# Optimization experiments

Hardware: AMD Instinct MI355X
Metric: run time of the kernel (lower is better)

## Reference

```python
import jax, jax.numpy as jnp
import numpy as np

NUM_LABELS = 64
START, END, PAD = 0, 1, 2
B, L, V, D = 128, 1024, 30000, 256


def make_transitions(key):
    # replicates CRF.init_weights
    t = jax.random.uniform(key, (NUM_LABELS, NUM_LABELS), minval=-0.1, maxval=0.1)
    t = t.at[:, START].set(-10000.0)
    t = t.at[END, :].set(-10000.0)
    t = t.at[PAD, :].set(-10000.0)
    t = t.at[:, PAD].set(-10000.0)
    t = t.at[PAD, PAD].set(0.0)
    t = t.at[PAD, END].set(0.0)
    return t.astype(jnp.float32)


def setup_inputs() -> dict:
    key = jax.random.key(0)
    k0, k1, k2, k3, k4 = jax.random.split(key, 5)
    x = jax.random.randint(k0, (B, L), 0, V)
    tags = jax.random.randint(k1, (B, L), 0, NUM_LABELS)
    mask = jnp.ones((B, L), dtype=jnp.float32)  # ignored by CRF (source passes mask=None)
    embed = jax.random.normal(k2, (V, D), dtype=jnp.float32)
    W = jax.random.normal(k3, (D, NUM_LABELS), dtype=jnp.float32) * 0.05
    b = jnp.zeros((NUM_LABELS,), dtype=jnp.float32)
    trans = make_transitions(k4)
    return {"x": x, "tags": tags, "mask": mask, "embed": embed, "W": W, "b": b, "trans": trans}


def _crf_nll(emissions, tags, trans):
    # emissions: [B, L, T]; tags: [B, L]; trans: [T, T]
    # NOTE: original CRF.forward ignores the user mask (passes mask=None ->
    # all-ones mask), so every position is valid and last tag is tags[:, -1].
    # gold path score
    e_scores = jnp.take_along_axis(emissions, tags[:, :, None], axis=2)[:, :, 0].sum(axis=1)
    t_scores = trans[tags[:, :-1], tags[:, 1:]].sum(axis=1)
    scores = e_scores + t_scores + trans[START, tags[:, 0]] + trans[tags[:, -1], END]
    # log partition: forward algorithm (log-space recursion over time)
    alpha0 = trans[START][None, :] + emissions[:, 0]  # [B, T]

    def step(alphas, emit_t):
        # alphas: [B, T_prev] -> logsumexp over previous tag
        new = jax.nn.logsumexp(alphas[:, :, None] + trans[None, :, :], axis=1) + emit_t
        return new, None

    alphas, _ = jax.lax.scan(step, alpha0, jnp.swapaxes(emissions[:, 1:], 0, 1))
    log_z = jax.nn.logsumexp(alphas + trans[:, END][None, :], axis=1)  # [B]
    return -jnp.sum(scores - log_z)


def reference(x, tags, mask, embed, W, b, trans):
    emissions = embed[x] @ W + b  # [B, L, T]
    return _crf_nll(emissions, tags, trans)
```

## Files before the change

### kernel.cpp

```cpp
#include <hip/hip_runtime.h>
#include <hip/hip_bf16.h>

#define B_ 128
#define L_ 1024
#define T_ 64
#define CSH 5
#define C_ 32

using short8 = __attribute__((ext_vector_type(8))) short;
using f32x4  = __attribute__((ext_vector_type(4))) float;
using f32x16 = __attribute__((ext_vector_type(16))) float;

static __device__ __forceinline__ unsigned short bfb(float x) {
  return __builtin_bit_cast(unsigned short, __float2bfloat16(x));
}
static __device__ __forceinline__ float asf(unsigned u) { return __builtin_bit_cast(float, u); }
static __device__ __forceinline__ float bf2f(unsigned short b) { return asf(((unsigned)b) << 16); }
static __device__ __forceinline__ unsigned pk2(float lo, float hi) {
  __hip_bfloat162 h = __float22bfloat162_rn(float2{lo, hi});
  unsigned u;
  __builtin_memcpy(&u, &h, 4);
  return u;
}
static __device__ __forceinline__ unsigned pk2t(float lo, float hi) {
  return __builtin_amdgcn_perm(__builtin_bit_cast(unsigned, hi),
                               __builtin_bit_cast(unsigned, lo), 0x07060302u);
}
static __device__ __forceinline__ void pswap(unsigned& x, unsigned& y) {
  asm("v_permlane32_swap_b32 %0, %1" : "+v"(x), "+v"(y));
}

__global__ __launch_bounds__(256) void k_prep(const float* __restrict__ W,
                                              unsigned short* __restrict__ Wswz,
                                              float* __restrict__ score,
                                              float* __restrict__ out) {
  if (blockIdx.x == 0) {
    if (threadIdx.x < 128) score[threadIdx.x] = 0.f;
    if (threadIdx.x == 0) out[0] = 0.f;
  }
  const int t = blockIdx.x * 256 + threadIdx.x;
  const int e = t * 4, k = e >> 6, n0 = e & 63;
  float4 w4 = *(const float4*)(W + e);
  const int base = ((k >> 5) << 11) + ((n0 >> 4) << 9) + (((k >> 3) & 3) << 7) +
                   ((n0 & 15) << 3) + (k & 7);
  Wswz[base + 0]  = bfb(w4.x);
  Wswz[base + 8]  = bfb(w4.y);
  Wswz[base + 16] = bfb(w4.z);
  Wswz[base + 24] = bfb(w4.w);
}

__global__ __launch_bounds__(256) void k_scan(const int* __restrict__ x,
                                              const int* __restrict__ tags,
                                              const float* __restrict__ embed,
                                              const unsigned short* __restrict__ Wswz,
                                              const float* __restrict__ bias,
                                              const float* __restrict__ trans,
                                              uint4* __restrict__ XT,
                                              float* __restrict__ rlog,
                                              float* __restrict__ score) {
  __shared__ __align__(16) unsigned short Ftile[4][2048];
  const int wv = threadIdx.x >> 6, L = threadIdx.x & 63;
  const int job = blockIdx.x * 4 + wv;
  const int c = job & (C_ - 1);
  const int b = job >> CSH;
  const int K = (1023 + C_ - 1) >> CSH;
  const int a = 1 + c * K;
  const int len = min(K, 1024 - a);
  const int nh = L & 31, hh = L >> 5;
  const int m = L & 15, q = L >> 4;
  unsigned short* Ft = Ftile[wv];
  const int* tg = tags + (size_t)b * L_;

  const float bj0 = bias[m], bj1 = bias[16 + m], bj2 = bias[32 + m], bj3 = bias[48 + m];
  for (int p = 0; p < 2; p++) {
    int tok = a + 16 * p + m;
    if (tok > 1023) tok = 1023;
    const float* er = embed + (size_t)x[b * 1024 + tok] * 256;
    f32x4 acc[4] = {{0.f,0.f,0.f,0.f},{0.f,0.f,0.f,0.f},{0.f,0.f,0.f,0.f},{0.f,0.f,0.f,0.f}};
#pragma unroll
    for (int kap = 0; kap < 8; kap++) {
      float4 p0 = *(const float4*)(er + 32 * kap + 8 * q);
      float4 p1 = *(const float4*)(er + 32 * kap + 8 * q + 4);
      unsigned u0 = pk2(p0.x, p0.y), u1 = pk2(p0.z, p0.w);
      unsigned u2 = pk2(p1.x, p1.y), u3 = pk2(p1.z, p1.w);
      short8 af = __builtin_bit_cast(short8, make_uint4(u0, u1, u2, u3));
#pragma unroll
      for (int u = 0; u < 4; u++) {
        short8 bf8 = *(const short8*)&Wswz[kap * 2048 + u * 512 + q * 128 + m * 8];
        acc[u] = __builtin_amdgcn_mfma_f32_16x16x32_bf16(af, bf8, acc[u], 0, 0, 0);
      }
    }
#pragma unroll
    for (int r = 0; r < 4; r++) {
      float e0 = acc[0][r] + bj0, e1 = acc[1][r] + bj1;
      float e2 = acc[2][r] + bj2, e3 = acc[3][r] + bj3;
      float mr = fmaxf(fmaxf(e0, e1), fmaxf(e2, e3));
#pragma unroll
      for (int off = 1; off < 16; off <<= 1) mr = fmaxf(mr, __shfl_xor(mr, off));
      float x0 = __expf(e0 - mr), x1 = __expf(e1 - mr);
      float x2 = __expf(e2 - mr), x3 = __expf(e3 - mr);
      float sr = (x0 + x1) + (x2 + x3);
#pragma unroll
      for (int off = 1; off < 16; off <<= 1) sr += __shfl_xor(sr, off);
      float rs = 1.0f / sr;
      const int row = 16 * p + 4 * q + r;
      Ft[row * 64 + m]      = bfb(x0 * rs);
      Ft[row * 64 + 16 + m] = bfb(x1 * rs);
      Ft[row * 64 + 32 + m] = bfb(x2 * rs);
      Ft[row * 64 + 48 + m] = bfb(x3 * rs);
    }
  }
  {
    float gold = 0.f;
    if (L < len) {
      const int tga = tg[a + L], tgp = tg[a - 1 + L];
      gold = __logf(bf2f(Ft[L * 64 + tga])) + trans[tgp * T_ + tga];
    }
#pragma unroll
    for (int off = 1; off < 64; off <<= 1) gold += __shfl_xor(gold, off);
    if (L == 0) atomicAdd(&score[b], gold);
  }

  short8 Af[2][4];
#pragma unroll
  for (int I = 0; I < 2; I++)
#pragma unroll
    for (int kap = 0; kap < 4; kap++) {
      short8 aa;
#pragma unroll
      for (int d = 0; d < 8; d++) {
        const int k = 16 * kap + 8 * hh + d;
        aa[d] = (short)bfb(__expf(trans[k * T_ + 32 * I + nh]));
      }
      Af[I][kap] = aa;
    }
  unsigned Bf[4][2][4];
#pragma unroll
  for (int kap = 0; kap < 4; kap++)
#pragma unroll
    for (int J = 0; J < 2; J++)
#pragma unroll
      for (int dw = 0; dw < 4; dw++) {
        int k0 = 16 * kap + 8 * hh + 2 * dw, n = 32 * J + nh;
        unsigned u = 0;
        if (k0 == n) u = 0x3F80u;
        if (k0 + 1 == n) u = 0x3F800000u;
        Bf[kap][J][dw] = u;
      }

  float logacc = 0.f;
  const f32x16 Z = {};
  for (int s = 0; s < len; s++) {
    uint2 Fc[2][4];
#pragma unroll
    for (int I = 0; I < 2; I++)
#pragma unroll
      for (int j = 0; j < 4; j++)
        Fc[I][j] = *(const uint2*)&Ft[s * 64 + (16 * I + 4 * j + 2 * hh) * 2];
    const bool rn = ((s & 15) == 15);
    float rs = 1.0f;
#pragma unroll
    for (int J = 0; J < 2; J++) {
      f32x16 D[2];
#pragma unroll
      for (int I = 0; I < 2; I++) {
        short8 b0 = __builtin_bit_cast(short8,
            make_uint4(Bf[0][J][0], Bf[0][J][1], Bf[0][J][2], Bf[0][J][3]));
        f32x16 d = __builtin_amdgcn_mfma_f32_32x32x16_bf16(Af[I][0], b0, Z, 0, 0, 0);
#pragma unroll
        for (int kap = 1; kap < 4; kap++) {
          short8 bk = __builtin_bit_cast(short8,
              make_uint4(Bf[kap][J][0], Bf[kap][J][1], Bf[kap][J][2], Bf[kap][J][3]));
          d = __builtin_amdgcn_mfma_f32_32x32x16_bf16(Af[I][kap], bk, d, 0, 0, 0);
        }
        D[I] = d;
      }
#pragma unroll
      for (int I = 0; I < 2; I++)
#pragma unroll
        for (int j = 0; j < 4; j++) {
          uint2 g = Fc[I][j];
          float f0 = asf(g.x << 16), f1 = asf(g.x & 0xffff0000u);
          float f2 = asf(g.y << 16), f3 = asf(g.y & 0xffff0000u);
          D[I][4 * j + 0] *= f0;
          D[I][4 * j + 1] *= f1;
          D[I][4 * j + 2] *= f2;
          D[I][4 * j + 3] *= f3;
        }
      if (rn) {
        if (J == 0) {
          float mx = D[0][0];
#pragma unroll
          for (int I = 0; I < 2; I++)
#pragma unroll
            for (int r = 0; r < 16; r++) mx = fmaxf(mx, D[I][r]);
#pragma unroll
          for (int off = 1; off < 64; off <<= 1) mx = fmaxf(mx, __shfl_xor(mx, off));
          rs = 1.0f / mx;
          logacc += __logf(mx);
        }
#pragma unroll
        for (int I = 0; I < 2; I++)
#pragma unroll
          for (int r = 0; r < 16; r++) D[I][r] *= rs;
      }
      unsigned PDt[2][4][2];
#pragma unroll
      for (int I = 0; I < 2; I++)
#pragma unroll
        for (int j = 0; j < 4; j++) {
          PDt[I][j][0] = pk2t(D[I][4 * j + 0], D[I][4 * j + 1]);
          PDt[I][j][1] = pk2t(D[I][4 * j + 2], D[I][4 * j + 3]);
        }
#pragma unroll
      for (int kap = 0; kap < 4; kap++) {
        const int Ip = kap >> 1, e2 = 2 * (kap & 1);
        unsigned x0 = PDt[Ip][e2][0], y0 = PDt[Ip][e2 + 1][0];
        unsigned x1 = PDt[Ip][e2][1], y1 = PDt[Ip][e2 + 1][1];
        pswap(x0, y0);
        pswap(x1, y1);
        Bf[kap][J][0] = x0;
        Bf[kap][J][1] = x1;
        Bf[kap][J][2] = y0;
        Bf[kap][J][3] = y1;
      }
    }
  }
  {
    uint4* Xj = XT + (size_t)job * 512 + L;
#pragma unroll
    for (int J = 0; J < 2; J++)
#pragma unroll
      for (int kap = 0; kap < 4; kap++)
        Xj[(J * 4 + kap) * 64] =
            make_uint4(Bf[kap][J][0], Bf[kap][J][1], Bf[kap][J][2], Bf[kap][J][3]);
  }
  if (L == 0) rlog[job] = logacc;
}

__global__ __launch_bounds__(256) void k_tail(const uint4* __restrict__ XT,
                                              const float* __restrict__ rlog,
                                              const float* __restrict__ score,
                                              const int* __restrict__ x,
                                              const float* __restrict__ embed,
                                              const float* __restrict__ W,
                                              const float* __restrict__ bias,
                                              const float* __restrict__ trans,
                                              const int* __restrict__ tags,
                                              float* __restrict__ out) {
  __shared__ __align__(16) unsigned short Ptile[4][4096];
  __shared__ __align__(16) float vS[64];
  __shared__ float tlg[4];
  const int wv = threadIdx.x >> 6, L = threadIdx.x & 63;
  const int b = blockIdx.x;
  const int nh = L & 31, hh = L >> 5;
  const int* tg = tags + (size_t)b * L_;
  const f32x16 Z = {};
  unsigned Bf[4][2][4];

  const uint4* Sb4 = XT + ((size_t)(b * C_ + 8 * wv)) * 512 + L;
  {
    float plog = 0.f;
#pragma unroll
    for (int kap = 0; kap < 4; kap++)
#pragma unroll
      for (int J = 0; J < 2; J++)
#pragma unroll
        for (int dw = 0; dw < 4; dw++) {
          int k0 = 16 * kap + 8 * hh + 2 * dw, n = 32 * J + nh;
          unsigned u = 0;
          if (k0 == n) u = 0x3F80u;
          if (k0 + 1 == n) u = 0x3F800000u;
          Bf[kap][J][dw] = u;
        }
    uint4 Aq[2][4], Aqn[2][4];
#pragma unroll
    for (int I = 0; I < 2; I++)
#pragma unroll
      for (int kap = 0; kap < 4; kap++)
        Aq[I][kap] = Sb4[7 * 512 + (I * 4 + kap) * 64];
    for (int rr = 0; rr < 8; rr++) {
      const int r = 7 - rr;
      if (r > 0) {
#pragma unroll
        for (int I = 0; I < 2; I++)
#pragma unroll
          for (int kap = 0; kap < 4; kap++)
            Aqn[I][kap] = Sb4[(size_t)(r - 1) * 512 + (I * 4 + kap) * 64];
      }
      short8 Ap[2][4];
#pragma unroll
      for (int I = 0; I < 2; I++)
#pragma unroll
        for (int kap = 0; kap < 4; kap++)
          Ap[I][kap] = __builtin_bit_cast(short8, Aq[I][kap]);
      const bool last = (r == 0);
      float rsw = 1.0f;
#pragma unroll
      for (int J = 0; J < 2; J++) {
        f32x16 D[2];
#pragma unroll
        for (int I = 0; I < 2; I++) {
          short8 b0 = __builtin_bit_cast(short8,
              make_uint4(Bf[0][J][0], Bf[0][J][1], Bf[0][J][2], Bf[0][J][3]));
          f32x16 d = __builtin_amdgcn_mfma_f32_32x32x16_bf16(Ap[I][0], b0, Z, 0, 0, 0);
#pragma unroll
          for (int kap = 1; kap < 4; kap++) {
            short8 bk = __builtin_bit_cast(short8,
                make_uint4(Bf[kap][J][0], Bf[kap][J][1], Bf[kap][J][2], Bf[kap][J][3]));
            d = __builtin_amdgcn_mfma_f32_32x32x16_bf16(Ap[I][kap], bk, d, 0, 0, 0);
          }
          D[I] = d;
        }
        if (J == 0) {
          float mx = D[0][0];
#pragma unroll
          for (int I = 0; I < 2; I++)
#pragma unroll
            for (int rr2 = 0; rr2 < 16; rr2++) mx = fmaxf(mx, D[I][rr2]);
#pragma unroll
          for (int off = 1; off < 64; off <<= 1) mx = fmaxf(mx, __shfl_xor(mx, off));
          mx = fmaxf(mx, 1e-30f);
          rsw = 1.0f / mx;
          plog += __logf(mx);
        }
#pragma unroll
        for (int I = 0; I < 2; I++)
#pragma unroll
          for (int rr2 = 0; rr2 < 16; rr2++) D[I][rr2] *= rsw;
        unsigned PDt[2][4][2];
#pragma unroll
        for (int I = 0; I < 2; I++)
#pragma unroll
          for (int j = 0; j < 4; j++) {
            PDt[I][j][0] = pk2t(D[I][4 * j + 0], D[I][4 * j + 1]);
            PDt[I][j][1] = pk2t(D[I][4 * j + 2], D[I][4 * j + 3]);
          }
        if (last) {
          unsigned short* Xrow = Ptile[wv] + 32 * J + nh;
#pragma unroll
          for (int I = 0; I < 2; I++)
#pragma unroll
            for (int j = 0; j < 4; j++)
#pragma unroll
              for (int pp = 0; pp < 2; pp++) {
                const int rw = 32 * I + 8 * j + 4 * hh + 2 * pp;
                Xrow[rw * 64] = (unsigned short)(PDt[I][j][pp] & 0xffffu);
                Xrow[(rw + 1) * 64] = (unsigned short)(PDt[I][j][pp] >> 16);
              }
        } else {
#pragma unroll
          for (int kap = 0; kap < 4; kap++) {
            const int Ip = kap >> 1, e2 = 2 * (kap & 1);
            unsigned x0 = PDt[Ip][e2][0], y0 = PDt[Ip][e2 + 1][0];
            unsigned x1 = PDt[Ip][e2][1], y1 = PDt[Ip][e2 + 1][1];
            pswap(x0, y0);
            pswap(x1, y1);
            Bf[kap][J][0] = x0;
            Bf[kap][J][1] = x1;
            Bf[kap][J][2] = y0;
            Bf[kap][J][3] = y1;
          }
        }
      }
      if (r > 0) {
#pragma unroll
        for (int I = 0; I < 2; I++)
#pragma unroll
          for (int kap = 0; kap < 4; kap++)
            Aq[I][kap] = Aqn[I][kap];
      }
    }
    if (L == 0) tlg[wv] = plog;
  }
  __syncthreads();
  if (threadIdx.x >= 64) return;

  float tlog = (tlg[0] + tlg[1]) + (tlg[2] + tlg[3]);

  const int i = L;
  const float* er0 = embed + (size_t)x[(size_t)b * L_] * 256;
  float e0 = bias[i], e1 = 0.f, e2 = 0.f, e3 = 0.f;
#pragma unroll 16
  for (int d = 0; d < 256; d += 4) {
    e0 = fmaf(er0[d + 0], W[(d + 0) * T_ + i], e0);
    e1 = fmaf(er0[d + 1], W[(d + 1) * T_ + i], e1);
    e2 = fmaf(er0[d + 2], W[(d + 2) * T_ + i], e2);
    e3 = fmaf(er0[d + 3], W[(d + 3) * T_ + i], e3);
  }
  float e = (e0 + e1) + (e2 + e3);
  float mr = e;
#pragma unroll
  for (int off = 1; off < 64; off <<= 1) mr = fmaxf(mr, __shfl_xor(mr, off));
  float pex = __expf(e - mr);
  float sr = pex;
#pragma unroll
  for (int off = 1; off < 64; off <<= 1) sr += __shfl_xor(sr, off);
  const int t0 = tg[0];
  float sc = score[b];
  sc += (__shfl(e, t0) - mr) - __logf(sr);
  sc += trans[t0] + trans[tg[L_ - 1] * T_ + 1];
  vS[i] = __expf(trans[i]) * (pex / sr);
  float rl = (i < 32) ? rlog[b * C_ + i] : 0.f;
#pragma unroll
  for (int off = 1; off < 64; off <<= 1) rl += __shfl_xor(rl, off);

  float tacc = 0.f;
  {
#pragma unroll
    for (int kap = 0; kap < 4; kap++)
#pragma unroll
      for (int J = 0; J < 2; J++)
#pragma unroll
        for (int dw = 0; dw < 4; dw++) {
          int k0 = 16 * kap + 8 * hh + 2 * dw, n = 32 * J + nh;
          unsigned u = 0;
          if (k0 == n) u = 0x3F80u;
          if (k0 + 1 == n) u = 0x3F800000u;
          Bf[kap][J][dw] = u;
        }
    for (int rr = 0; rr < 4; rr++) {
      const int r = 3 - rr;
      short8 Ap[2][4];
#pragma unroll
      for (int I = 0; I < 2; I++)
#pragma unroll
        for (int kap = 0; kap < 4; kap++)
          Ap[I][kap] = *(const short8*)&Ptile[r][(32 * I + nh) * 64 + 16 * kap + 8 * hh];
      const bool last = (r == 0);
      float rsw = 1.0f;
#pragma unroll
      for (int J = 0; J < 2; J++) {
        f32x16 D[2];
#pragma unroll
        for (int I = 0; I < 2; I++) {
          short8 b0 = __builtin_bit_cast(short8,
              make_uint4(Bf[0][J][0], Bf[0][J][1], Bf[0][J][2], Bf[0][J][3]));
          f32x16 d = __builtin_amdgcn_mfma_f32_32x32x16_bf16(Ap[I][0], b0, Z, 0, 0, 0);
#pragma unroll
          for (int kap = 1; kap < 4; kap++) {
            short8 bk = __builtin_bit_cast(short8,
                make_uint4(Bf[kap][J][0], Bf[kap][J][1], Bf[kap][J][2], Bf[kap][J][3]));
            d = __builtin_amdgcn_mfma_f32_32x32x16_bf16(Ap[I][kap], bk, d, 0, 0, 0);
          }
          D[I] = d;
        }
        if (J == 0) {
          float mx = D[0][0];
#pragma unroll
          for (int I = 0; I < 2; I++)
#pragma unroll
            for (int rr2 = 0; rr2 < 16; rr2++) mx = fmaxf(mx, D[I][rr2]);
#pragma unroll
          for (int off = 1; off < 64; off <<= 1) mx = fmaxf(mx, __shfl_xor(mx, off));
          mx = fmaxf(mx, 1e-30f);
          rsw = 1.0f / mx;
          tlog += __logf(mx);
        }
#pragma unroll
        for (int I = 0; I < 2; I++)
#pragma unroll
          for (int rr2 = 0; rr2 < 16; rr2++) D[I][rr2] *= rsw;
        if (last) {
          float dJ = 0.f;
#pragma unroll
          for (int I = 0; I < 2; I++)
#pragma unroll
            for (int r2 = 0; r2 < 16; r2++)
              dJ = fmaf(D[I][r2], vS[32 * I + (r2 & 3) + 8 * (r2 >> 2) + 4 * hh], dJ);
          tacc = fmaf(__expf(trans[(32 * J + nh) * T_ + 1]), dJ, tacc);
        } else {
          unsigned PDt[2][4][2];
#pragma unroll
          for (int I = 0; I < 2; I++)
#pragma unroll
            for (int j = 0; j < 4; j++) {
              PDt[I][j][0] = pk2t(D[I][4 * j + 0], D[I][4 * j + 1]);
              PDt[I][j][1] = pk2t(D[I][4 * j + 2], D[I][4 * j + 3]);
            }
#pragma unroll
          for (int kap = 0; kap < 4; kap++) {
            const int Ip = kap >> 1, e2b = 2 * (kap & 1);
            unsigned x0 = PDt[Ip][e2b][0], y0 = PDt[Ip][e2b + 1][0];
            unsigned x1 = PDt[Ip][e2b][1], y1 = PDt[Ip][e2b + 1][1];
            pswap(x0, y0);
            pswap(x1, y1);
            Bf[kap][J][0] = x0;
            Bf[kap][J][1] = x1;
            Bf[kap][J][2] = y0;
            Bf[kap][J][3] = y1;
          }
        }
      }
    }
  }
  float t2 = tacc;
#pragma unroll
  for (int off = 1; off < 64; off <<= 1) t2 += __shfl_xor(t2, off);
  if (i == 0) {
    const float logz = rl + tlog + __logf(t2);
    atomicAdd(out, -(sc - logz));
  }
}

extern "C" void kernel_launch(void* const* d_in, const int* in_sizes, int n_in,
                              void* d_out, int out_size, void* d_ws, size_t ws_size,
                              hipStream_t stream) {
  const int* x = (const int*)d_in[0];
  const int* tags = (const int*)d_in[1];
  const float* embed = (const float*)d_in[3];
  const float* W = (const float*)d_in[4];
  const float* bias = (const float*)d_in[5];
  const float* trans = (const float*)d_in[6];

  char* ws = (char*)d_ws;
  uint4* XT = (uint4*)ws;
  float* rlog = (float*)(ws + (size_t)C_ * 1048576);
  float* score = (float*)((char*)rlog + 4096 * 4);
  unsigned short* Wswz = (unsigned short*)((char*)score + 128 * 4);
  float* out = (float*)d_out;

  k_prep<<<16, 256, 0, stream>>>(W, Wswz, score, out);
  k_scan<<<32 * C_, 256, 0, stream>>>(x, tags, embed, Wswz, bias, trans, XT, rlog, score);
  k_tail<<<B_, 256, 0, stream>>>(XT, rlog, score, x, embed, W, bias, trans, tags, out);
}
```

Measured before the change: 191.7 us.

## Split each scan chunk across two waves by output column half

Each chunk job of the forward-algorithm matrix chain now runs on a 128-thread block with two waves. Each wave computes one 32-column half of the 64x64 product, where before a single wave did both halves serially. The emission tile is built cooperatively, one 16-token half per wave. The periodic renormalisation scale is shared through LDS with a block barrier every 16 steps. This halves the per-wave serial MFMA chain length and doubles the number of waves, at the cost of barrier synchronisation and some duplicated work per wave.

Result: no change. 192.3 us (+0.3%).

```diff
diff --git a/kernel.cpp b/kernel.cpp
--- a/kernel.cpp
+++ b/kernel.cpp
@@ -49,7 +49,7 @@
   Wswz[base + 24] = bfb(w4.w);
 }
 
-__global__ __launch_bounds__(256) void k_scan(const int* __restrict__ x,
+__global__ __launch_bounds__(128) void k_scan(const int* __restrict__ x,
                                               const int* __restrict__ tags,
                                               const float* __restrict__ embed,
                                               const unsigned short* __restrict__ Wswz,
@@ -58,9 +58,10 @@
                                               uint4* __restrict__ XT,
                                               float* __restrict__ rlog,
                                               float* __restrict__ score) {
-  __shared__ __align__(16) unsigned short Ftile[4][2048];
+  __shared__ __align__(16) unsigned short Ftile[2048];
+  __shared__ float rsx[2];
   const int wv = threadIdx.x >> 6, L = threadIdx.x & 63;
-  const int job = blockIdx.x * 4 + wv;
+  const int job = blockIdx.x;
   const int c = job & (C_ - 1);
   const int b = job >> CSH;
   const int K = (1023 + C_ - 1) >> CSH;
@@ -68,11 +69,12 @@
   const int len = min(K, 1024 - a);
   const int nh = L & 31, hh = L >> 5;
   const int m = L & 15, q = L >> 4;
-  unsigned short* Ft = Ftile[wv];
+  unsigned short* Ft = Ftile;
   const int* tg = tags + (size_t)b * L_;
 
   const float bj0 = bias[m], bj1 = bias[16 + m], bj2 = bias[32 + m], bj3 = bias[48 + m];
-  for (int p = 0; p < 2; p++) {
+  {
+    const int p = wv;
     int tok = a + 16 * p + m;
     if (tok > 1023) tok = 1023;
     const float* er = embed + (size_t)x[b * 1024 + tok] * 256;
@@ -110,7 +112,8 @@
       Ft[row * 64 + 48 + m] = bfb(x3 * rs);
     }
   }
-  {
+  __syncthreads();
+  if (wv == 0) {
     float gold = 0.f;
     if (L < len) {
       const int tga = tg[a + L], tgp = tg[a - 1 + L];
@@ -134,19 +137,17 @@
       }
       Af[I][kap] = aa;
     }
-  unsigned Bf[4][2][4];
+  unsigned Bf[4][4];
 #pragma unroll
   for (int kap = 0; kap < 4; kap++)
 #pragma unroll
-    for (int J = 0; J < 2; J++)
-#pragma unroll
-      for (int dw = 0; dw < 4; dw++) {
-        int k0 = 16 * kap + 8 * hh + 2 * dw, n = 32 * J + nh;
-        unsigned u = 0;
-        if (k0 == n) u = 0x3F80u;
-        if (k0 + 1 == n) u = 0x3F800000u;
-        Bf[kap][J][dw] = u;
-      }
+    for (int dw = 0; dw < 4; dw++) {
+      int k0 = 16 * kap + 8 * hh + 2 * dw, n = 32 * wv + nh;
+      unsigned u = 0;
+      if (k0 == n) u = 0x3F80u;
+      if (k0 + 1 == n) u = 0x3F800000u;
+      Bf[kap][dw] = u;
+    }
 
   float logacc = 0.f;
   const f32x16 Z = {};
@@ -158,84 +159,80 @@
       for (int j = 0; j < 4; j++)
         Fc[I][j] = *(const uint2*)&Ft[s * 64 + (16 * I + 4 * j + 2 * hh) * 2];
     const bool rn = ((s & 15) == 15);
-    float rs = 1.0f;
-#pragma unroll
-    for (int J = 0; J < 2; J++) {
-      f32x16 D[2];
-#pragma unroll
-      for (int I = 0; I < 2; I++) {
-        short8 b0 = __builtin_bit_cast(short8,
-            make_uint4(Bf[0][J][0], Bf[0][J][1], Bf[0][J][2], Bf[0][J][3]));
-        f32x16 d = __builtin_amdgcn_mfma_f32_32x32x16_bf16(Af[I][0], b0, Z, 0, 0, 0);
-#pragma unroll
-        for (int kap = 1; kap < 4; kap++) {
-          short8 bk = __builtin_bit_cast(short8,
-              make_uint4(Bf[kap][J][0], Bf[kap][J][1], Bf[kap][J][2], Bf[kap][J][3]));
-          d = __builtin_amdgcn_mfma_f32_32x32x16_bf16(Af[I][kap], bk, d, 0, 0, 0);
-        }
-        D[I] = d;
-      }
+    f32x16 D[2];
+#pragma unroll
+    for (int I = 0; I < 2; I++) {
+      short8 b0 = __builtin_bit_cast(short8,
+          make_uint4(Bf[0][0], Bf[0][1], Bf[0][2], Bf[0][3]));
+      f32x16 d = __builtin_amdgcn_mfma_f32_32x32x16_bf16(Af[I][0], b0, Z, 0, 0, 0);
+#pragma unroll
+      for (int kap = 1; kap < 4; kap++) {
+        short8 bk = __builtin_bit_cast(short8,
+            make_uint4(Bf[kap][0], Bf[kap][1], Bf[kap][2], Bf[kap][3]));
+        d = __builtin_amdgcn_mfma_f32_32x32x16_bf16(Af[I][kap], bk, d, 0, 0, 0);
+      }
+      D[I] = d;
+    }
+#pragma unroll
+    for (int I = 0; I < 2; I++)
+#pragma unroll
+      for (int j = 0; j < 4; j++) {
+        uint2 g = Fc[I][j];
+        float f0 = asf(g.x << 16), f1 = asf(g.x & 0xffff0000u);
+        float f2 = asf(g.y << 16), f3 = asf(g.y & 0xffff0000u);
+        D[I][4 * j + 0] *= f0;
+        D[I][4 * j + 1] *= f1;
+        D[I][4 * j + 2] *= f2;
+        D[I][4 * j + 3] *= f3;
+      }
+    if (rn) {
+      if (wv == 0) {
+        float mx = D[0][0];
+#pragma unroll
+        for (int I = 0; I < 2; I++)
+#pragma unroll
+          for (int r = 0; r < 16; r++) mx = fmaxf(mx, D[I][r]);
+#pragma unroll
+        for (int off = 1; off < 64; off <<= 1) mx = fmaxf(mx, __shfl_xor(mx, off));
+        logacc += __logf(mx);
+        rsx[(s >> 4) & 1] = 1.0f / mx;
+      }
+      __syncthreads();
+      const float rs = rsx[(s >> 4) & 1];
 #pragma unroll
       for (int I = 0; I < 2; I++)
 #pragma unroll
-        for (int j = 0; j < 4; j++) {
-          uint2 g = Fc[I][j];
-          float f0 = asf(g.x << 16), f1 = asf(g.x & 0xffff0000u);
-          float f2 = asf(g.y << 16), f3 = asf(g.y & 0xffff0000u);
-          D[I][4 * j + 0] *= f0;
-          D[I][4 * j + 1] *= f1;
-          D[I][4 * j + 2] *= f2;
-          D[I][4 * j + 3] *= f3;
-        }
-      if (rn) {
-        if (J == 0) {
-          float mx = D[0][0];
-#pragma unroll
-          for (int I = 0; I < 2; I++)
-#pragma unroll
-            for (int r = 0; r < 16; r++) mx = fmaxf(mx, D[I][r]);
-#pragma unroll
-          for (int off = 1; off < 64; off <<= 1) mx = fmaxf(mx, __shfl_xor(mx, off));
-          rs = 1.0f / mx;
-          logacc += __logf(mx);
-        }
-#pragma unroll
-        for (int I = 0; I < 2; I++)
-#pragma unroll
-          for (int r = 0; r < 16; r++) D[I][r] *= rs;
-      }
-      unsigned PDt[2][4][2];
-#pragma unroll
-      for (int I = 0; I < 2; I++)
-#pragma unroll
-        for (int j = 0; j < 4; j++) {
-          PDt[I][j][0] = pk2t(D[I][4 * j + 0], D[I][4 * j + 1]);
-          PDt[I][j][1] = pk2t(D[I][4 * j + 2], D[I][4 * j + 3]);
-        }
-#pragma unroll
-      for (int kap = 0; kap < 4; kap++) {
-        const int Ip = kap >> 1, e2 = 2 * (kap & 1);
-        unsigned x0 = PDt[Ip][e2][0], y0 = PDt[Ip][e2 + 1][0];
-        unsigned x1 = PDt[Ip][e2][1], y1 = PDt[Ip][e2 + 1][1];
-        pswap(x0, y0);
-        pswap(x1, y1);
-        Bf[kap][J][0] = x0;
-        Bf[kap][J][1] = x1;
-        Bf[kap][J][2] = y0;
-        Bf[kap][J][3] = y1;
-      }
+        for (int r = 0; r < 16; r++) D[I][r] *= rs;
+    }
+    unsigned PDt[2][4][2];
+#pragma unroll
+    for (int I = 0; I < 2; I++)
+#pragma unroll
+      for (int j = 0; j < 4; j++) {
+        PDt[I][j][0] = pk2t(D[I][4 * j + 0], D[I][4 * j + 1]);
+        PDt[I][j][1] = pk2t(D[I][4 * j + 2], D[I][4 * j + 3]);
+      }
+#pragma unroll
+    for (int kap = 0; kap < 4; kap++) {
+      const int Ip = kap >> 1, e2 = 2 * (kap & 1);
+      unsigned x0 = PDt[Ip][e2][0], y0 = PDt[Ip][e2 + 1][0];
+      unsigned x1 = PDt[Ip][e2][1], y1 = PDt[Ip][e2 + 1][1];
+      pswap(x0, y0);
+      pswap(x1, y1);
+      Bf[kap][0] = x0;
+      Bf[kap][1] = x1;
+      Bf[kap][2] = y0;
+      Bf[kap][3] = y1;
     }
   }
   {
     uint4* Xj = XT + (size_t)job * 512 + L;
 #pragma unroll
-    for (int J = 0; J < 2; J++)
-#pragma unroll
-      for (int kap = 0; kap < 4; kap++)
-        Xj[(J * 4 + kap) * 64] =
-            make_uint4(Bf[kap][J][0], Bf[kap][J][1], Bf[kap][J][2], Bf[kap][J][3]);
-  }
-  if (L == 0) rlog[job] = logacc;
+    for (int kap = 0; kap < 4; kap++)
+      Xj[(wv * 4 + kap) * 64] =
+          make_uint4(Bf[kap][0], Bf[kap][1], Bf[kap][2], Bf[kap][3]);
+  }
+  if (wv == 0 && L == 0) rlog[job] = logacc;
 }
 
 __global__ __launch_bounds__(256) void k_tail(const uint4* __restrict__ XT,
@@ -521,6 +518,6 @@
   float* out = (float*)d_out;
 
   k_prep<<<16, 256, 0, stream>>>(W, Wswz, score, out);
-  k_scan<<<32 * C_, 256, 0, stream>>>(x, tags, embed, Wswz, bias, trans, XT, rlog, score);
+  k_scan<<<B_ * C_, 128, 0, stream>>>(x, tags, embed, Wswz, bias, trans, XT, rlog, score);
   k_tail<<<B_, 256, 0, stream>>>(XT, rlog, score, x, embed, W, bias, trans, tags, out);
 }
```

## Process two independent chunk scans per wavefront to interleave MFMA chains

Applied to the files above, without the earlier changes.

Each wavefront now handles two adjacent time chunks of the same sequence instead of one, interleaving their serial MFMA transfer-matrix recurrences in one loop. The two independent dependency chains are meant to hide MFMA and conversion latency in the latency-bound scan, and the grid shrinks by half. In exchange it roughly doubles register pressure, which may reduce occupancy or cause spills, and it adds a predicate for the shorter final chunk.

Result: slower. 238.0 us (+24.1%).

```diff
diff --git a/kernel.cpp b/kernel.cpp
--- a/kernel.cpp
+++ b/kernel.cpp
@@ -58,63 +58,73 @@
                                               uint4* __restrict__ XT,
                                               float* __restrict__ rlog,
                                               float* __restrict__ score) {
-  __shared__ __align__(16) unsigned short Ftile[4][2048];
+  __shared__ __align__(16) unsigned short Ftile[4][2][2048];
   const int wv = threadIdx.x >> 6, L = threadIdx.x & 63;
-  const int job = blockIdx.x * 4 + wv;
-  const int c = job & (C_ - 1);
-  const int b = job >> CSH;
-  const int K = (1023 + C_ - 1) >> CSH;
-  const int a = 1 + c * K;
-  const int len = min(K, 1024 - a);
+  const int job0 = blockIdx.x * 8 + wv * 2;
+  const int job1 = job0 + 1;
+  const int c0 = job0 & (C_ - 1);
+  const int b = job0 >> CSH;
+  const int a0 = 1 + c0 * 32, a1 = a0 + 32;
+  const int len1 = min(32, 1024 - a1);
   const int nh = L & 31, hh = L >> 5;
   const int m = L & 15, q = L >> 4;
-  unsigned short* Ft = Ftile[wv];
+  unsigned short* Ft0 = Ftile[wv][0];
+  unsigned short* Ft1 = Ftile[wv][1];
   const int* tg = tags + (size_t)b * L_;
 
   const float bj0 = bias[m], bj1 = bias[16 + m], bj2 = bias[32 + m], bj3 = bias[48 + m];
-  for (int p = 0; p < 2; p++) {
-    int tok = a + 16 * p + m;
-    if (tok > 1023) tok = 1023;
-    const float* er = embed + (size_t)x[b * 1024 + tok] * 256;
-    f32x4 acc[4] = {{0.f,0.f,0.f,0.f},{0.f,0.f,0.f,0.f},{0.f,0.f,0.f,0.f},{0.f,0.f,0.f,0.f}};
-#pragma unroll
-    for (int kap = 0; kap < 8; kap++) {
-      float4 p0 = *(const float4*)(er + 32 * kap + 8 * q);
-      float4 p1 = *(const float4*)(er + 32 * kap + 8 * q + 4);
-      unsigned u0 = pk2(p0.x, p0.y), u1 = pk2(p0.z, p0.w);
-      unsigned u2 = pk2(p1.x, p1.y), u3 = pk2(p1.z, p1.w);
-      short8 af = __builtin_bit_cast(short8, make_uint4(u0, u1, u2, u3));
-#pragma unroll
-      for (int u = 0; u < 4; u++) {
-        short8 bf8 = *(const short8*)&Wswz[kap * 2048 + u * 512 + q * 128 + m * 8];
-        acc[u] = __builtin_amdgcn_mfma_f32_16x16x32_bf16(af, bf8, acc[u], 0, 0, 0);
-      }
-    }
-#pragma unroll
-    for (int r = 0; r < 4; r++) {
-      float e0 = acc[0][r] + bj0, e1 = acc[1][r] + bj1;
-      float e2 = acc[2][r] + bj2, e3 = acc[3][r] + bj3;
-      float mr = fmaxf(fmaxf(e0, e1), fmaxf(e2, e3));
-#pragma unroll
-      for (int off = 1; off < 16; off <<= 1) mr = fmaxf(mr, __shfl_xor(mr, off));
-      float x0 = __expf(e0 - mr), x1 = __expf(e1 - mr);
-      float x2 = __expf(e2 - mr), x3 = __expf(e3 - mr);
-      float sr = (x0 + x1) + (x2 + x3);
-#pragma unroll
-      for (int off = 1; off < 16; off <<= 1) sr += __shfl_xor(sr, off);
-      float rs = 1.0f / sr;
-      const int row = 16 * p + 4 * q + r;
-      Ft[row * 64 + m]      = bfb(x0 * rs);
-      Ft[row * 64 + 16 + m] = bfb(x1 * rs);
-      Ft[row * 64 + 32 + m] = bfb(x2 * rs);
-      Ft[row * 64 + 48 + m] = bfb(x3 * rs);
+#pragma unroll
+  for (int jb = 0; jb < 2; jb++) {
+    unsigned short* Ftj = jb ? Ft1 : Ft0;
+    const int aj = jb ? a1 : a0;
+    for (int p = 0; p < 2; p++) {
+      int tok = aj + 16 * p + m;
+      if (tok > 1023) tok = 1023;
+      const float* er = embed + (size_t)x[b * 1024 + tok] * 256;
+      f32x4 acc[4] = {{0.f,0.f,0.f,0.f},{0.f,0.f,0.f,0.f},{0.f,0.f,0.f,0.f},{0.f,0.f,0.f,0.f}};
+#pragma unroll
+      for (int kap = 0; kap < 8; kap++) {
+        float4 p0 = *(const float4*)(er + 32 * kap + 8 * q);
+        float4 p1 = *(const float4*)(er + 32 * kap + 8 * q + 4);
+        unsigned u0 = pk2(p0.x, p0.y), u1 = pk2(p0.z, p0.w);
+        unsigned u2 = pk2(p1.x, p1.y), u3 = pk2(p1.z, p1.w);
+        short8 af = __builtin_bit_cast(short8, make_uint4(u0, u1, u2, u3));
+#pragma unroll
+        for (int u = 0; u < 4; u++) {
+          short8 bf8 = *(const short8*)&Wswz[kap * 2048 + u * 512 + q * 128 + m * 8];
+          acc[u] = __builtin_amdgcn_mfma_f32_16x16x32_bf16(af, bf8, acc[u], 0, 0, 0);
+        }
+      }
+#pragma unroll
+      for (int r = 0; r < 4; r++) {
+        float e0 = acc[0][r] + bj0, e1 = acc[1][r] + bj1;
+        float e2 = acc[2][r] + bj2, e3 = acc[3][r] + bj3;
+        float mr = fmaxf(fmaxf(e0, e1), fmaxf(e2, e3));
+#pragma unroll
+        for (int off = 1; off < 16; off <<= 1) mr = fmaxf(mr, __shfl_xor(mr, off));
+        float x0 = __expf(e0 - mr), x1 = __expf(e1 - mr);
+        float x2 = __expf(e2 - mr), x3 = __expf(e3 - mr);
+        float sr = (x0 + x1) + (x2 + x3);
+#pragma unroll
+        for (int off = 1; off < 16; off <<= 1) sr += __shfl_xor(sr, off);
+        float rs = 1.0f / sr;
+        const int row = 16 * p + 4 * q + r;
+        Ftj[row * 64 + m]      = bfb(x0 * rs);
+        Ftj[row * 64 + 16 + m] = bfb(x1 * rs);
+        Ftj[row * 64 + 32 + m] = bfb(x2 * rs);
+        Ftj[row * 64 + 48 + m] = bfb(x3 * rs);
+      }
     }
   }
   {
     float gold = 0.f;
-    if (L < len) {
-      const int tga = tg[a + L], tgp = tg[a - 1 + L];
-      gold = __logf(bf2f(Ft[L * 64 + tga])) + trans[tgp * T_ + tga];
+    if (L < 32) {
+      const int tga = tg[a0 + L], tgp = tg[a0 - 1 + L];
+      gold += __logf(bf2f(Ft0[L * 64 + tga])) + trans[tgp * T_ + tga];
+    }
+    if (L < len1) {
+      const int tga = tg[a1 + L], tgp = tg[a1 - 1 + L];
+      gold += __logf(bf2f(Ft1[L * 64 + tga])) + trans[tgp * T_ + tga];
     }
 #pragma unroll
     for (int off = 1; off < 64; off <<= 1) gold += __shfl_xor(gold, off);
@@ -134,7 +144,7 @@
       }
       Af[I][kap] = aa;
     }
-  unsigned Bf[4][2][4];
+  unsigned Bf0[4][2][4], Bf1[4][2][4];
 #pragma unroll
   for (int kap = 0; kap < 4; kap++)
 #pragma unroll
@@ -145,97 +155,180 @@
         unsigned u = 0;
         if (k0 == n) u = 0x3F80u;
         if (k0 + 1 == n) u = 0x3F800000u;
-        Bf[kap][J][dw] = u;
-      }
-
-  float logacc = 0.f;
+        Bf0[kap][J][dw] = u;
+        Bf1[kap][J][dw] = u;
+      }
+
+  float logacc0 = 0.f, logacc1 = 0.f;
   const f32x16 Z = {};
-  for (int s = 0; s < len; s++) {
-    uint2 Fc[2][4];
+  for (int s = 0; s < 32; s++) {
+    const bool do1 = (s < len1);
+    const bool rn = ((s & 15) == 15);
+    uint2 Fc0[2][4], Fc1[2][4];
 #pragma unroll
     for (int I = 0; I < 2; I++)
 #pragma unroll
       for (int j = 0; j < 4; j++)
-        Fc[I][j] = *(const uint2*)&Ft[s * 64 + (16 * I + 4 * j + 2 * hh) * 2];
-    const bool rn = ((s & 15) == 15);
-    float rs = 1.0f;
+        Fc0[I][j] = *(const uint2*)&Ft0[s * 64 + (16 * I + 4 * j + 2 * hh) * 2];
+    if (do1) {
+#pragma unroll
+      for (int I = 0; I < 2; I++)
+#pragma unroll
+        for (int j = 0; j < 4; j++)
+          Fc1[I][j] = *(const uint2*)&Ft1[s * 64 + (16 * I + 4 * j + 2 * hh) * 2];
+    }
+    float rs0 = 1.0f, rs1 = 1.0f;
 #pragma unroll
     for (int J = 0; J < 2; J++) {
-      f32x16 D[2];
+      short8 bk0[4], bk1[4];
+#pragma unroll
+      for (int kap = 0; kap < 4; kap++)
+        bk0[kap] = __builtin_bit_cast(short8,
+            make_uint4(Bf0[kap][J][0], Bf0[kap][J][1], Bf0[kap][J][2], Bf0[kap][J][3]));
+      if (do1) {
+#pragma unroll
+        for (int kap = 0; kap < 4; kap++)
+          bk1[kap] = __builtin_bit_cast(short8,
+              make_uint4(Bf1[kap][J][0], Bf1[kap][J][1], Bf1[kap][J][2], Bf1[kap][J][3]));
+      }
+      f32x16 D0[2], D1[2];
 #pragma unroll
       for (int I = 0; I < 2; I++) {
-        short8 b0 = __builtin_bit_cast(short8,
-            make_uint4(Bf[0][J][0], Bf[0][J][1], Bf[0][J][2], Bf[0][J][3]));
-        f32x16 d = __builtin_amdgcn_mfma_f32_32x32x16_bf16(Af[I][0], b0, Z, 0, 0, 0);
-#pragma unroll
-        for (int kap = 1; kap < 4; kap++) {
-          short8 bk = __builtin_bit_cast(short8,
-              make_uint4(Bf[kap][J][0], Bf[kap][J][1], Bf[kap][J][2], Bf[kap][J][3]));
-          d = __builtin_amdgcn_mfma_f32_32x32x16_bf16(Af[I][kap], bk, d, 0, 0, 0);
-        }
-        D[I] = d;
+        f32x16 d = __builtin_amdgcn_mfma_f32_32x32x16_bf16(Af[I][0], bk0[0], Z, 0, 0, 0);
+#pragma unroll
+        for (int kap = 1; kap < 4; kap++)
+          d = __builtin_amdgcn_mfma_f32_32x32x16_bf16(Af[I][kap], bk0[kap], d, 0, 0, 0);
+        D0[I] = d;
+      }
+      if (do1) {
+#pragma unroll
+        for (int I = 0; I < 2; I++) {
+          f32x16 d = __builtin_amdgcn_mfma_f32_32x32x16_bf16(Af[I][0], bk1[0], Z, 0, 0, 0);
+#pragma unroll
+          for (int kap = 1; kap < 4; kap++)
+            d = __builtin_amdgcn_mfma_f32_32x32x16_bf16(Af[I][kap], bk1[kap], d, 0, 0, 0);
+          D1[I] = d;
+        }
       }
 #pragma unroll
       for (int I = 0; I < 2; I++)
 #pragma unroll
         for (int j = 0; j < 4; j++) {
-          uint2 g = Fc[I][j];
-          float f0 = asf(g.x << 16), f1 = asf(g.x & 0xffff0000u);
-          float f2 = asf(g.y << 16), f3 = asf(g.y & 0xffff0000u);
-          D[I][4 * j + 0] *= f0;
-          D[I][4 * j + 1] *= f1;
-          D[I][4 * j + 2] *= f2;
-          D[I][4 * j + 3] *= f3;
-        }
+          uint2 g = Fc0[I][j];
+          D0[I][4 * j + 0] *= asf(g.x << 16);
+          D0[I][4 * j + 1] *= asf(g.x & 0xffff0000u);
+          D0[I][4 * j + 2] *= asf(g.y << 16);
+          D0[I][4 * j + 3] *= asf(g.y & 0xffff0000u);
+        }
+      if (do1) {
+#pragma unroll
+        for (int I = 0; I < 2; I++)
+#pragma unroll
+          for (int j = 0; j < 4; j++) {
+            uint2 g = Fc1[I][j];
+            D1[I][4 * j + 0] *= asf(g.x << 16);
+            D1[I][4 * j + 1] *= asf(g.x & 0xffff0000u);
+            D1[I][4 * j + 2] *= asf(g.y << 16);
+            D1[I][4 * j + 3] *= asf(g.y & 0xffff0000u);
+          }
+      }
       if (rn) {
         if (J == 0) {
-          float mx = D[0][0];
+          float mx0 = D0[0][0];
 #pragma unroll
           for (int I = 0; I < 2; I++)
 #pragma unroll
-            for (int r = 0; r < 16; r++) mx = fmaxf(mx, D[I][r]);
-#pragma unroll
-          for (int off = 1; off < 64; off <<= 1) mx = fmaxf(mx, __shfl_xor(mx, off));
-          rs = 1.0f / mx;
-          logacc += __logf(mx);
-        }
-#pragma unroll
-        for (int I = 0; I < 2; I++)
-#pragma unroll
-          for (int r = 0; r < 16; r++) D[I][r] *= rs;
-      }
-      unsigned PDt[2][4][2];
-#pragma unroll
-      for (int I = 0; I < 2; I++)
-#pragma unroll
-        for (int j = 0; j < 4; j++) {
-          PDt[I][j][0] = pk2t(D[I][4 * j + 0], D[I][4 * j + 1]);
-          PDt[I][j][1] = pk2t(D[I][4 * j + 2], D[I][4 * j + 3]);
-        }
+            for (int r = 0; r < 16; r++) mx0 = fmaxf(mx0, D0[I][r]);
+#pragma unroll
+          for (int off = 1; off < 64; off <<= 1) mx0 = fmaxf(mx0, __shfl_xor(mx0, off));
+          rs0 = 1.0f / mx0;
+          logacc0 += __logf(mx0);
+          if (do1) {
+            float mx1 = D1[0][0];
+#pragma unroll
+            for (int I = 0; I < 2; I++)
+#pragma unroll
+              for (int r = 0; r < 16; r++) mx1 = fmaxf(mx1, D1[I][r]);
+#pragma unroll
+            for (int off = 1; off < 64; off <<= 1) mx1 = fmaxf(mx1, __shfl_xor(mx1, off));
+            rs1 = 1.0f / mx1;
+            logacc1 += __logf(mx1);
+          }
+        }
+#pragma unroll
+        for (int I = 0; I < 2; I++)
+#pragma unroll
+          for (int r = 0; r < 16; r++) D0[I][r] *= rs0;
+        if (do1) {
+#pragma unroll
+          for (int I = 0; I < 2; I++)
+#pragma unroll
+            for (int r = 0; r < 16; r++) D1[I][r] *= rs1;
+        }
+      }
+      {
+        unsigned PDt[2][4][2];
+#pragma unroll
+        for (int I = 0; I < 2; I++)
+#pragma unroll
+          for (int j = 0; j < 4; j++) {
+            PDt[I][j][0] = pk2t(D0[I][4 * j + 0], D0[I][4 * j + 1]);
+            PDt[I][j][1] = pk2t(D0[I][4 * j + 2], D0[I][4 * j + 3]);
+          }
+#pragma unroll
+        for (int kap = 0; kap < 4; kap++) {
+          const int Ip = kap >> 1, e2 = 2 * (kap & 1);
+          unsigned x0 = PDt[Ip][e2][0], y0 = PDt[Ip][e2 + 1][0];
+          unsigned x1 = PDt[Ip][e2][1], y1 = PDt[Ip][e2 + 1][1];
+          pswap(x0, y0);
+          pswap(x1, y1);
+          Bf0[kap][J][0] = x0;
+          Bf0[kap][J][1] = x1;
+          Bf0[kap][J][2] = y0;
+          Bf0[kap][J][3] = y1;
+        }
+      }
+      if (do1) {
+        unsigned PDt[2][4][2];
+#pragma unroll
+        for (int I = 0; I < 2; I++)
+#pragma unroll
+          for (int j = 0; j < 4; j++) {
+            PDt[I][j][0] = pk2t(D1[I][4 * j + 0], D1[I][4 * j + 1]);
+            PDt[I][j][1] = pk2t(D1[I][4 * j + 2], D1[I][4 * j + 3]);
+          }
+#pragma unroll
+        for (int kap = 0; kap < 4; kap++) {
+          const int Ip = kap >> 1, e2 = 2 * (kap & 1);
+          unsigned x0 = PDt[Ip][e2][0], y0 = PDt[Ip][e2 + 1][0];
+          unsigned x1 = PDt[Ip][e2][1], y1 = PDt[Ip][e2 + 1][1];
+          pswap(x0, y0);
+          pswap(x1, y1);
+          Bf1[kap][J][0] = x0;
+          Bf1[kap][J][1] = x1;
+          Bf1[kap][J][2] = y0;
+          Bf1[kap][J][3] = y1;
+        }
+      }
+    }
+  }
+  {
+    uint4* Xj0 = XT + (size_t)job0 * 512 + L;
+    uint4* Xj1 = XT + (size_t)job1 * 512 + L;
+#pragma unroll
+    for (int J = 0; J < 2; J++)
 #pragma unroll
       for (int kap = 0; kap < 4; kap++) {
-        const int Ip = kap >> 1, e2 = 2 * (kap & 1);
-        unsigned x0 = PDt[Ip][e2][0], y0 = PDt[Ip][e2 + 1][0];
-        unsigned x1 = PDt[Ip][e2][1], y1 = PDt[Ip][e2 + 1][1];
-        pswap(x0, y0);
-        pswap(x1, y1);
-        Bf[kap][J][0] = x0;
-        Bf[kap][J][1] = x1;
-        Bf[kap][J][2] = y0;
-        Bf[kap][J][3] = y1;
-      }
-    }
-  }
-  {
-    uint4* Xj = XT + (size_t)job * 512 + L;
-#pragma unroll
-    for (int J = 0; J < 2; J++)
-#pragma unroll
-      for (int kap = 0; kap < 4; kap++)
-        Xj[(J * 4 + kap) * 64] =
-            make_uint4(Bf[kap][J][0], Bf[kap][J][1], Bf[kap][J][2], Bf[kap][J][3]);
-  }
-  if (L == 0) rlog[job] = logacc;
+        Xj0[(J * 4 + kap) * 64] =
+            make_uint4(Bf0[kap][J][0], Bf0[kap][J][1], Bf0[kap][J][2], Bf0[kap][J][3]);
+        Xj1[(J * 4 + kap) * 64] =
+            make_uint4(Bf1[kap][J][0], Bf1[kap][J][1], Bf1[kap][J][2], Bf1[kap][J][3]);
+      }
+  }
+  if (L == 0) {
+    rlog[job0] = logacc0;
+    rlog[job1] = logacc1;
+  }
 }
 
 __global__ __launch_bounds__(256) void k_tail(const uint4* __restrict__ XT,
@@ -521,6 +614,6 @@
   float* out = (float*)d_out;
 
   k_prep<<<16, 256, 0, stream>>>(W, Wswz, score, out);
-  k_scan<<<32 * C_, 256, 0, stream>>>(x, tags, embed, Wswz, bias, trans, XT, rlog, score);
+  k_scan<<<B_ * C_ / 8, 256, 0, stream>>>(x, tags, embed, Wswz, bias, trans, XT, rlog, score);
   k_tail<<<B_, 256, 0, stream>>>(XT, rlog, score, x, embed, W, bias, trans, tags, out);
 }
```
